# Optimization experiments

Measured on AMD Instinct MI355X. Metric: run time of the kernel, lower is better.

The kernel has to match this reference:

```python
import jax, jax.numpy as jnp
import numpy as np

L, B, D = 512, 32, 256  # seq_len, batch (hardcoded 32 in source), in_size == hidden_size
H = D


def setup_inputs() -> dict:
    key = jax.random.key(0)
    ks = jax.random.split(key, 9)
    s_in = 1.0 / np.sqrt(D)
    s_h = 1.0 / np.sqrt(H)
    return {
        "v": jax.random.normal(ks[0], (L, B, D), jnp.float32),
        "h0": jax.random.normal(ks[1], (B, H), jnp.float32),       # torch.randn h
        "Vvec": jax.random.normal(ks[2], (B, H), jnp.float32),     # torch.randn V (squeezed [B,H,1])
        "Wp": jax.random.normal(ks[3], (H, D), jnp.float32) * s_in,   # nn.Linear(D,H,bias=False).weight
        "Wp_": jax.random.normal(ks[4], (H, D), jnp.float32) * s_in,
        "W_ih": jax.random.normal(ks[5], (3 * H, D), jnp.float32) * s_h,  # GRUCell weight_ih
        "W_hh": jax.random.normal(ks[6], (3 * H, H), jnp.float32) * s_h,
        "b_ih": jax.random.normal(ks[7], (3 * H,), jnp.float32) * s_h,
        "b_hh": jax.random.normal(ks[8], (3 * H,), jnp.float32) * s_h,
    }


def _gru_cell(c, h, W_ih, W_hh, b_ih, b_hh):
    # torch.nn.GRUCell math
    gi = c @ W_ih.T + b_ih   # [B, 3H]
    gh = h @ W_hh.T + b_hh   # [B, 3H]
    i_r, i_z, i_n = jnp.split(gi, 3, axis=1)
    h_r, h_z, h_n = jnp.split(gh, 3, axis=1)
    r = jax.nn.sigmoid(i_r + h_r)
    z = jax.nn.sigmoid(i_z + h_z)
    n = jnp.tanh(i_n + r * h_n)
    return (1.0 - z) * n + z * h


def reference(v, h0, Vvec, Wp, Wp_, W_ih, W_hh, b_ih, b_hh):
    # Hoist the two linear projections out of the scan (they don't depend on h).
    xq = jnp.einsum('lbd,hd->lbh', v, Wp)    # Wp(v[i]) for all i
    xv = jnp.einsum('lbd,hd->lbh', v, Wp_)   # Wp_(v), reused every step

    def step(h, xq_i):
        x = jnp.tanh(xq_i[None, :, :] + xv)          # [L, B, H]
        s = jnp.einsum('lbh,bh->bl', x, Vvec)        # attention scores over L
        a = jax.nn.softmax(s, axis=1)                # [B, L]
        c = jnp.einsum('bl,lbd->bd', a, v)           # context [B, D]
        h_new = _gru_cell(c, h, W_ih, W_hh, b_ih, b_hh)
        return h_new, h_new

    _, hs = jax.lax.scan(step, h0, xq)  # hs: [L, B, H]
    # dropout is identity in eval mode
    return hs
```

## Files before the change

kernel.cpp:

```cpp
#include <hip/hip_runtime.h>
#include <stdint.h>


#define C2    2.8853900817779268f
#define LOG2E 1.4426950408889634f

typedef __fp16 f16x2 __attribute__((ext_vector_type(2)));
typedef __fp16 f16x4_t __attribute__((ext_vector_type(4)));
typedef __fp16 f16x8 __attribute__((ext_vector_type(8)));
typedef float f32x4 __attribute__((ext_vector_type(4)));

static __device__ __forceinline__ float rcp_f(float x)  { return __builtin_amdgcn_rcpf(x); }
static __device__ __forceinline__ float exp2_f(float x) { return __builtin_amdgcn_exp2f(x); }
#if __has_builtin(__builtin_amdgcn_rcph)
static __device__ __forceinline__ __fp16 rcph(__fp16 x) {
  return (__fp16)__builtin_amdgcn_rcph((_Float16)x);
}
#else
static __device__ __forceinline__ __fp16 rcph(__fp16 x) {
  return (__fp16)__builtin_amdgcn_rcpf((float)x);
}
#endif
static __device__ __forceinline__ float dot2f(f16x2 a, f16x2 b, float c) {
  return __builtin_amdgcn_fdot2(a, b, c, false);
}
static __device__ __forceinline__ f16x8 cvt8(float4 a, float4 b) {
  f16x8 f;
  f[0] = (__fp16)a.x; f[1] = (__fp16)a.y; f[2] = (__fp16)a.z; f[3] = (__fp16)a.w;
  f[4] = (__fp16)b.x; f[5] = (__fp16)b.y; f[6] = (__fp16)b.z; f[7] = (__fp16)b.w;
  return f;
}


__global__ __launch_bounds__(256) void proj_k(
    const float* __restrict__ v, const float* __restrict__ Wp,
    const float* __restrict__ Wp_, __fp16* __restrict__ Eq,
    __fp16* __restrict__ Ev)
{
  __shared__ __align__(16) __fp16 As[64][40];
  __shared__ __align__(16) __fp16 Wqs[64][40];
  __shared__ __align__(16) __fp16 Wvs[64][40];
  const int t = threadIdx.x, wave = t >> 6, lane = t & 63;
  const int quad = lane >> 4, col = lane & 15;
  const int n0 = blockIdx.x * 64, m0 = blockIdx.y * 64;
  const int srow = t >> 2, skq = t & 3;

  f32x4 accq[4], accv[4];
#pragma unroll
  for (int nt = 0; nt < 4; ++nt) {
    accq[nt] = (f32x4){0.f, 0.f, 0.f, 0.f};
    accv[nt] = (f32x4){0.f, 0.f, 0.f, 0.f};
  }

  for (int kc = 0; kc < 8; ++kc) {
    const int k0 = kc * 32;
    {
      const float4* ap = (const float4*)&v[(size_t)(m0 + srow) * 256 + k0 + skq * 8];
      *(f16x8*)&As[srow][skq * 8] = cvt8(ap[0], ap[1]);
      const float4* qp = (const float4*)&Wp[(size_t)(n0 + srow) * 256 + k0 + skq * 8];
      *(f16x8*)&Wqs[srow][skq * 8] = cvt8(qp[0], qp[1]);
      const float4* vp = (const float4*)&Wp_[(size_t)(n0 + srow) * 256 + k0 + skq * 8];
      *(f16x8*)&Wvs[srow][skq * 8] = cvt8(vp[0], vp[1]);
    }
    __syncthreads();
    f16x8 a = *(const f16x8*)&As[wave * 16 + col][quad * 8];
#pragma unroll
    for (int nt = 0; nt < 4; ++nt) {
      f16x8 bq = *(const f16x8*)&Wqs[nt * 16 + col][quad * 8];
      f16x8 bv = *(const f16x8*)&Wvs[nt * 16 + col][quad * 8];
      accq[nt] = __builtin_amdgcn_mfma_f32_16x16x32_f16(a, bq, accq[nt], 0, 0, 0);
      accv[nt] = __builtin_amdgcn_mfma_f32_16x16x32_f16(a, bv, accv[nt], 0, 0, 0);
    }
    __syncthreads();
  }

#pragma unroll
  for (int nt = 0; nt < 4; ++nt)
#pragma unroll
    for (int r = 0; r < 4; ++r) {
      size_t m = m0 + wave * 16 + quad * 4 + r;
      size_t n = n0 + nt * 16 + col;
      float eq = C2 * accq[nt][r], ev = C2 * accv[nt][r];
      eq = fminf(fmaxf(eq, -14.f), 15.5f);
      ev = fminf(fmaxf(ev, -14.f), 15.5f);
      Eq[m * 256 + n] = (__fp16)exp2_f(eq);
      Ev[m * 256 + n] = (__fp16)exp2_f(ev);
    }
}

__global__ __launch_bounds__(256) void score_k(
    const __fp16* __restrict__ Eq, const __fp16* __restrict__ Ev,
    const float* __restrict__ Vvec, float* __restrict__ S)
{
  __shared__ __align__(16) __fp16 Eqs[64][72];
  __shared__ __align__(16) __fp16 Evs[32][72];
  __shared__ __align__(16) __fp16 Vs[256];
  const int t = threadIdx.x;
  const int tx = t & 15, ty = t >> 4;
  const int l0 = blockIdx.x * 32;
  const int i0 = blockIdx.y * 64;
  const int b  = blockIdx.z;

  Vs[t] = (__fp16)(-2.0f * Vvec[b * 256 + t]);
  float acc[4][2] = {};
  const f16x2 one2 = {(__fp16)1.f, (__fp16)1.f};

  for (int st = 0; st < 4; ++st) {
    const int h0 = st * 64;
#pragma unroll
    for (int s = 0; s < 2; ++s) {
      int f = t + s * 256;
      int row = f >> 3, cq = f & 7;
      *(f16x8*)&Eqs[row][cq * 8] =
          *(const f16x8*)&Eq[((size_t)(i0 + row) * 32 + b) * 256 + h0 + cq * 8];
    }
    {
      int row = t >> 3, cq = t & 7;
      *(f16x8*)&Evs[row][cq * 8] =
          *(const f16x8*)&Ev[((size_t)(l0 + row) * 32 + b) * 256 + h0 + cq * 8];
    }
    __syncthreads();

#pragma unroll
    for (int k8 = 0; k8 < 8; ++k8) {
      f16x8 vh8 = *(const f16x8*)&Vs[h0 + k8 * 8];
      f16x8 ev80 = *(const f16x8*)&Evs[tx][k8 * 8];
      f16x8 ev81 = *(const f16x8*)&Evs[tx + 16][k8 * 8];
      f16x8 eq8[4];
#pragma unroll
      for (int r = 0; r < 4; ++r)
        eq8[r] = *(const f16x8*)&Eqs[ty * 4 + r][k8 * 8];
#pragma unroll
      for (int q = 0; q < 4; ++q) {
        f16x2 vh2 = {vh8[q * 2], vh8[q * 2 + 1]};
        f16x2 e0  = {ev80[q * 2], ev80[q * 2 + 1]};
        f16x2 e1  = {ev81[q * 2], ev81[q * 2 + 1]};
#pragma unroll
        for (int r = 0; r < 4; ++r) {
          f16x2 eq2 = {eq8[r][q * 2], eq8[r][q * 2 + 1]};
          f16x2 d0 = eq2 * e0 + one2;
          f16x2 d1 = eq2 * e1 + one2;
          f16x2 r0 = {rcph(d0[0]), rcph(d0[1])};
          f16x2 r1 = {rcph(d1[0]), rcph(d1[1])};
          acc[r][0] = dot2f(vh2, r0, acc[r][0]);
          acc[r][1] = dot2f(vh2, r1, acc[r][1]);
        }
      }
    }
    __syncthreads();
  }

#pragma unroll
  for (int r = 0; r < 4; ++r) {
    float* ps = &S[((size_t)b * 512 + i0 + ty * 4 + r) * 512 + l0];
    ps[tx]      = acc[r][0];
    ps[tx + 16] = acc[r][1];
  }
}

__global__ __launch_bounds__(256) void softmax_k(float* __restrict__ S)
{
  const int wave = threadIdx.x >> 6, lane = threadIdx.x & 63;
  float* row = &S[((size_t)blockIdx.x * 4 + wave) * 512];
  float4 x0 = *(float4*)&row[lane * 4];
  float4 x1 = *(float4*)&row[256 + lane * 4];
  float m = fmaxf(fmaxf(fmaxf(x0.x, x0.y), fmaxf(x0.z, x0.w)),
                  fmaxf(fmaxf(x1.x, x1.y), fmaxf(x1.z, x1.w)));
#pragma unroll
  for (int o = 32; o; o >>= 1) m = fmaxf(m, __shfl_xor(m, o, 64));
  x0.x = exp2_f(LOG2E * (x0.x - m)); x0.y = exp2_f(LOG2E * (x0.y - m));
  x0.z = exp2_f(LOG2E * (x0.z - m)); x0.w = exp2_f(LOG2E * (x0.w - m));
  x1.x = exp2_f(LOG2E * (x1.x - m)); x1.y = exp2_f(LOG2E * (x1.y - m));
  x1.z = exp2_f(LOG2E * (x1.z - m)); x1.w = exp2_f(LOG2E * (x1.w - m));
  float sum = x0.x + x0.y + x0.z + x0.w + x1.x + x1.y + x1.z + x1.w;
#pragma unroll
  for (int o = 32; o; o >>= 1) sum += __shfl_xor(sum, o, 64);
  float inv = rcp_f(sum);
  x0.x *= inv; x0.y *= inv; x0.z *= inv; x0.w *= inv;
  x1.x *= inv; x1.y *= inv; x1.z *= inv; x1.w *= inv;
  *(float4*)&row[lane * 4] = x0;
  *(float4*)&row[256 + lane * 4] = x1;
}

__global__ __launch_bounds__(256) void ctxm_k(
    const float* __restrict__ Aw, const float* __restrict__ v,
    float* __restrict__ C)
{
  __shared__ __align__(16) __fp16 As[64][40];
  __shared__ __align__(16) __fp16 Vs[64][40];
  const int t = threadIdx.x, wave = t >> 6, lane = t & 63;
  const int quad = lane >> 4, col = lane & 15;
  const int d0 = blockIdx.x * 64, i0 = blockIdx.y * 64, b = blockIdx.z;
  const int srow = t >> 2, skq = t & 3;
  const int vl = t >> 3, vdq = t & 7;

  f32x4 acc[4];
#pragma unroll
  for (int nt = 0; nt < 4; ++nt) acc[nt] = (f32x4){0.f, 0.f, 0.f, 0.f};

  for (int kc = 0; kc < 16; ++kc) {
    const int l0 = kc * 32;
    {
      const float4* ap =
          (const float4*)&Aw[((size_t)b * 512 + i0 + srow) * 512 + l0 + skq * 8];
      *(f16x8*)&As[srow][skq * 8] = cvt8(ap[0], ap[1]);
      const float4* vp =
          (const float4*)&v[((size_t)(l0 + vl) * 32 + b) * 256 + d0 + vdq * 8];
      float4 v0 = vp[0], v1 = vp[1];
      float vv[8] = {v0.x, v0.y, v0.z, v0.w, v1.x, v1.y, v1.z, v1.w};
#pragma unroll
      for (int e = 0; e < 8; ++e) Vs[vdq * 8 + e][vl] = (__fp16)vv[e];
    }
    __syncthreads();
    f16x8 a = *(const f16x8*)&As[wave * 16 + col][quad * 8];
#pragma unroll
    for (int nt = 0; nt < 4; ++nt) {
      f16x8 bb = *(const f16x8*)&Vs[nt * 16 + col][quad * 8];
      acc[nt] = __builtin_amdgcn_mfma_f32_16x16x32_f16(a, bb, acc[nt], 0, 0, 0);
    }
    __syncthreads();
  }

#pragma unroll
  for (int nt = 0; nt < 4; ++nt)
#pragma unroll
    for (int r = 0; r < 4; ++r) {
      size_t i = i0 + wave * 16 + quad * 4 + r;
      size_t d = d0 + nt * 16 + col;
      C[(i * 32 + b) * 256 + d] = acc[nt][r];
    }
}

__global__ __launch_bounds__(256) void gi_k(
    const float* __restrict__ A, const float* __restrict__ W,
    const float* __restrict__ bih, const float* __restrict__ bhh,
    __fp16* __restrict__ G)
{
  __shared__ __align__(16) __fp16 As[64][40];
  __shared__ __align__(16) __fp16 Ws[64][40];
  const int t = threadIdx.x, wave = t >> 6, lane = t & 63;
  const int quad = lane >> 4, col = lane & 15;
  const int n0 = blockIdx.x * 64, m0 = blockIdx.y * 64;
  const int srow = t >> 2, skq = t & 3;

  f32x4 acc[4];
#pragma unroll
  for (int nt = 0; nt < 4; ++nt) acc[nt] = (f32x4){0.f, 0.f, 0.f, 0.f};

  for (int kc = 0; kc < 8; ++kc) {
    const int k0 = kc * 32;
    {
      const float4* ap = (const float4*)&A[(size_t)(m0 + srow) * 256 + k0 + skq * 8];
      *(f16x8*)&As[srow][skq * 8] = cvt8(ap[0], ap[1]);
      const float4* wp = (const float4*)&W[(size_t)(n0 + srow) * 256 + k0 + skq * 8];
      *(f16x8*)&Ws[srow][skq * 8] = cvt8(wp[0], wp[1]);
    }
    __syncthreads();
    f16x8 a = *(const f16x8*)&As[wave * 16 + col][quad * 8];
#pragma unroll
    for (int nt = 0; nt < 4; ++nt) {
      f16x8 b = *(const f16x8*)&Ws[nt * 16 + col][quad * 8];
      acc[nt] = __builtin_amdgcn_mfma_f32_16x16x32_f16(a, b, acc[nt], 0, 0, 0);
    }
    __syncthreads();
  }

#pragma unroll
  for (int nt = 0; nt < 4; ++nt) {
    int n = n0 + nt * 16 + col;
    float bias = bih[n] + (n < 512 ? bhh[n] : 0.f);
#pragma unroll
    for (int r = 0; r < 4; ++r) {
      size_t m = m0 + wave * 16 + quad * 4 + r;
      G[m * 768 + n] = (__fp16)(acc[nt][r] + bias);
    }
  }
}

__global__ __launch_bounds__(512, 1) void gru_k(
    const __fp16* __restrict__ Gi2, const float* __restrict__ Whh,
    const float* __restrict__ bhh, const float* __restrict__ h0,
    float* __restrict__ out)
{
  __shared__ __align__(16) __fp16 hA[2][256];
  const int t = threadIdx.x, wave = t >> 6, lane = t & 63;
  const int quad = lane >> 4, col = lane & 15;
  const int b = blockIdx.x;
  const int jw = wave * 32;

  f16x8 Bf[2][3][8];
#pragma unroll
  for (int p = 0; p < 2; ++p)
#pragma unroll
    for (int g = 0; g < 3; ++g) {
      const float* wrow = &Whh[(size_t)(g * 256 + jw + p * 16 + col) * 256];
#pragma unroll
      for (int kk = 0; kk < 8; ++kk) {
        const float4* wp = (const float4*)&wrow[kk * 32 + quad * 8];
        Bf[p][g][kk] = cvt8(wp[0], wp[1]);
      }
    }

  float hold[2];
  float bn[2];
#pragma unroll
  for (int p = 0; p < 2; ++p) {
    int j = jw + p * 16 + col;
    bn[p] = bhh[512 + j];
    float h = h0[(size_t)b * 256 + j];
    hold[p] = h;
    if (quad == 0) hA[0][j] = (__fp16)h;
  }
  __syncthreads();

  __fp16 gcur[2][3];
#pragma unroll
  for (int p = 0; p < 2; ++p)
#pragma unroll
    for (int g = 0; g < 3; ++g)
      gcur[p][g] = Gi2[(size_t)b * 768 + g * 256 + jw + p * 16 + col];

  for (int i = 0; i < 512; ++i) {
    __fp16 gnext[2][3];
    {
      int ip = (i + 1 < 512) ? (i + 1) : 511;
#pragma unroll
      for (int p = 0; p < 2; ++p)
#pragma unroll
        for (int g = 0; g < 3; ++g)
          gnext[p][g] =
              Gi2[(size_t)(ip * 32 + b) * 768 + g * 256 + jw + p * 16 + col];
    }

    f32x4 acc[2][3];
#pragma unroll
    for (int p = 0; p < 2; ++p)
#pragma unroll
      for (int g = 0; g < 3; ++g)
        acc[p][g] = (f32x4){0.f, 0.f, 0.f, 0.f};

    const __fp16* hbuf = hA[i & 1];
#pragma unroll
    for (int kk = 0; kk < 8; ++kk) {
      f16x8 a = *(const f16x8*)&hbuf[kk * 32 + quad * 8];
#pragma unroll
      for (int p = 0; p < 2; ++p)
#pragma unroll
        for (int g = 0; g < 3; ++g)
          acc[p][g] = __builtin_amdgcn_mfma_f32_16x16x32_f16(
              a, Bf[p][g][kk], acc[p][g], 0, 0, 0);
    }

    __fp16* hnext = hA[(i + 1) & 1];
#pragma unroll
    for (int p = 0; p < 2; ++p) {
      int j = jw + p * 16 + col;
      float rr = rcp_f(1.f + exp2_f(-LOG2E * ((float)gcur[p][0] + acc[p][0][0])));
      float zz = rcp_f(1.f + exp2_f(-LOG2E * ((float)gcur[p][1] + acc[p][1][0])));
      float na = fmaf(rr, acc[p][2][0] + bn[p], (float)gcur[p][2]);
      float nn = fmaf(-2.f, rcp_f(1.f + exp2_f(C2 * na)), 1.f);
      float h = fmaf(zz, hold[p] - nn, nn);
      hold[p] = h;
      if (quad == 0) {
        out[((size_t)i * 32 + b) * 256 + j] = h;
        hnext[j] = (__fp16)h;
      }
    }
#pragma unroll
    for (int p = 0; p < 2; ++p)
#pragma unroll
      for (int g = 0; g < 3; ++g) gcur[p][g] = gnext[p][g];
    __syncthreads();
  }
}

extern "C" void kernel_launch(void* const* d_in, const int* in_sizes, int n_in,
                              void* d_out, int out_size, void* d_ws, size_t ws_size,
                              hipStream_t stream)
{
  const float* v   = (const float*)d_in[0];
  const float* h0  = (const float*)d_in[1];
  const float* Vv  = (const float*)d_in[2];
  const float* Wp  = (const float*)d_in[3];
  const float* Wp_ = (const float*)d_in[4];
  const float* Wih = (const float*)d_in[5];
  const float* Whh = (const float*)d_in[6];
  const float* bih = (const float*)d_in[7];
  const float* bhh = (const float*)d_in[8];
  float* out = (float*)d_out;
  float* ws  = (float*)d_ws;

  __fp16* Eq = (__fp16*)ws;
  __fp16* Ev = (__fp16*)(ws + 4194304);
  float*  S  = ws + 8388608;
  float*  C  = ws;
  __fp16* Gi2 = (__fp16*)(ws + 4194304);

  proj_k<<<dim3(4, 256), 256, 0, stream>>>(v, Wp, Wp_, Eq, Ev);
  score_k<<<dim3(16, 8, 32), 256, 0, stream>>>(Eq, Ev, Vv, S);
  softmax_k<<<4096, 256, 0, stream>>>(S);
  ctxm_k<<<dim3(4, 8, 32), 256, 0, stream>>>(S, v, C);
  gi_k<<<dim3(12, 256), 256, 0, stream>>>(C, Wih, bih, bhh, Gi2);
  gru_k<<<32, 512, 0, stream>>>(Gi2, Whh, bhh, h0, out);
}
```

Before: 921.2 us.

## Fuse score, softmax and context matmul into one attention kernel

Replaces the separate score, softmax and context kernels with a single attn_k in which each block of 512 threads computes scores for 64 query rows against all 512 keys. It applies the softmax in registers with shuffles, stages the probabilities in fp16 shared memory, and runs the context MFMA matmul over the whole D. This removes the 32 MB fp32 score matrix round trip through global memory and two kernel launches, and the context is now written as fp16 for gi_k. The cost is a grid of only 256 blocks with launch_bounds(512,1), a heavy register load from 64 accumulators per thread, large shared memory and reduced occupancy.

```diff
diff --git a/kernel.cpp b/kernel.cpp
--- a/kernel.cpp
+++ b/kernel.cpp
@@ -6,7 +6,6 @@
 #define LOG2E 1.4426950408889634f
 
 typedef __fp16 f16x2 __attribute__((ext_vector_type(2)));
-typedef __fp16 f16x4_t __attribute__((ext_vector_type(4)));
 typedef __fp16 f16x8 __attribute__((ext_vector_type(8)));
 typedef float f32x4 __attribute__((ext_vector_type(4)));
 
@@ -88,62 +87,68 @@
     }
 }
 
-__global__ __launch_bounds__(256) void score_k(
+__global__ __launch_bounds__(512, 1) void attn_k(
     const __fp16* __restrict__ Eq, const __fp16* __restrict__ Ev,
-    const float* __restrict__ Vvec, float* __restrict__ S)
-{
-  __shared__ __align__(16) __fp16 Eqs[64][72];
-  __shared__ __align__(16) __fp16 Evs[32][72];
-  __shared__ __align__(16) __fp16 Vs[256];
+    const float* __restrict__ Vvec, const float* __restrict__ v,
+    __fp16* __restrict__ C)
+{
+  __shared__ __align__(16) __fp16 smem[43520];
+  __shared__ __align__(16) __fp16 Vsh[256];
   const int t = threadIdx.x;
-  const int tx = t & 15, ty = t >> 4;
-  const int l0 = blockIdx.x * 32;
-  const int i0 = blockIdx.y * 64;
-  const int b  = blockIdx.z;
-
-  Vs[t] = (__fp16)(-2.0f * Vvec[b * 256 + t]);
-  float acc[4][2] = {};
+  const int tx = t & 31, ty = t >> 5;
+  const int wave = t >> 6, lane = t & 63;
+  const int quad = lane >> 4, col = lane & 15;
+  const int i0 = blockIdx.x * 64, b = blockIdx.y;
+
+  if (t < 256) Vsh[t] = (__fp16)(-2.0f * Vvec[b * 256 + t]);
+
+  float acc[16][4];
+#pragma unroll
+  for (int lt = 0; lt < 16; ++lt)
+#pragma unroll
+    for (int r = 0; r < 4; ++r) acc[lt][r] = 0.f;
+
+  __fp16* Eqs = smem;
+  __fp16* Evs = smem + 4608;
   const f16x2 one2 = {(__fp16)1.f, (__fp16)1.f};
 
   for (int st = 0; st < 4; ++st) {
     const int h0 = st * 64;
-#pragma unroll
-    for (int s = 0; s < 2; ++s) {
-      int f = t + s * 256;
+    {
+      int row = t >> 3, cq = t & 7;
+      *(f16x8*)&Eqs[row * 72 + cq * 8] =
+          *(const f16x8*)&Eq[((size_t)(i0 + row) * 32 + b) * 256 + h0 + cq * 8];
+    }
+#pragma unroll
+    for (int s = 0; s < 8; ++s) {
+      int f = t + s * 512;
       int row = f >> 3, cq = f & 7;
-      *(f16x8*)&Eqs[row][cq * 8] =
-          *(const f16x8*)&Eq[((size_t)(i0 + row) * 32 + b) * 256 + h0 + cq * 8];
-    }
-    {
-      int row = t >> 3, cq = t & 7;
-      *(f16x8*)&Evs[row][cq * 8] =
-          *(const f16x8*)&Ev[((size_t)(l0 + row) * 32 + b) * 256 + h0 + cq * 8];
-    }
-    __syncthreads();
-
-#pragma unroll
-    for (int k8 = 0; k8 < 8; ++k8) {
-      f16x8 vh8 = *(const f16x8*)&Vs[h0 + k8 * 8];
-      f16x8 ev80 = *(const f16x8*)&Evs[tx][k8 * 8];
-      f16x8 ev81 = *(const f16x8*)&Evs[tx + 16][k8 * 8];
-      f16x8 eq8[4];
-#pragma unroll
-      for (int r = 0; r < 4; ++r)
-        eq8[r] = *(const f16x8*)&Eqs[ty * 4 + r][k8 * 8];
-#pragma unroll
-      for (int q = 0; q < 4; ++q) {
-        f16x2 vh2 = {vh8[q * 2], vh8[q * 2 + 1]};
-        f16x2 e0  = {ev80[q * 2], ev80[q * 2 + 1]};
-        f16x2 e1  = {ev81[q * 2], ev81[q * 2 + 1]};
-#pragma unroll
-        for (int r = 0; r < 4; ++r) {
-          f16x2 eq2 = {eq8[r][q * 2], eq8[r][q * 2 + 1]};
-          f16x2 d0 = eq2 * e0 + one2;
-          f16x2 d1 = eq2 * e1 + one2;
-          f16x2 r0 = {rcph(d0[0]), rcph(d0[1])};
-          f16x2 r1 = {rcph(d1[0]), rcph(d1[1])};
-          acc[r][0] = dot2f(vh2, r0, acc[r][0]);
-          acc[r][1] = dot2f(vh2, r1, acc[r][1]);
+      *(f16x8*)&Evs[row * 72 + cq * 8] =
+          *(const f16x8*)&Ev[((size_t)row * 32 + b) * 256 + h0 + cq * 8];
+    }
+    __syncthreads();
+
+#pragma unroll
+    for (int lt = 0; lt < 16; ++lt) {
+#pragma unroll
+      for (int k8 = 0; k8 < 8; ++k8) {
+        f16x8 vh8 = *(const f16x8*)&Vsh[h0 + k8 * 8];
+        f16x8 ev8 = *(const f16x8*)&Evs[(lt * 32 + tx) * 72 + k8 * 8];
+        f16x8 eq8[4];
+#pragma unroll
+        for (int r = 0; r < 4; ++r)
+          eq8[r] = *(const f16x8*)&Eqs[(ty * 4 + r) * 72 + k8 * 8];
+#pragma unroll
+        for (int q = 0; q < 4; ++q) {
+          f16x2 vh2 = {vh8[q * 2], vh8[q * 2 + 1]};
+          f16x2 e2  = {ev8[q * 2], ev8[q * 2 + 1]};
+#pragma unroll
+          for (int r = 0; r < 4; ++r) {
+            f16x2 eq2 = {eq8[r][q * 2], eq8[r][q * 2 + 1]};
+            f16x2 d = eq2 * e2 + one2;
+            f16x2 rr = {rcph(d[0]), rcph(d[1])};
+            acc[lt][r] = dot2f(vh2, rr, acc[lt][r]);
+          }
         }
       }
     }
@@ -152,87 +157,75 @@
 
 #pragma unroll
   for (int r = 0; r < 4; ++r) {
-    float* ps = &S[((size_t)b * 512 + i0 + ty * 4 + r) * 512 + l0];
-    ps[tx]      = acc[r][0];
-    ps[tx + 16] = acc[r][1];
-  }
-}
-
-__global__ __launch_bounds__(256) void softmax_k(float* __restrict__ S)
-{
-  const int wave = threadIdx.x >> 6, lane = threadIdx.x & 63;
-  float* row = &S[((size_t)blockIdx.x * 4 + wave) * 512];
-  float4 x0 = *(float4*)&row[lane * 4];
-  float4 x1 = *(float4*)&row[256 + lane * 4];
-  float m = fmaxf(fmaxf(fmaxf(x0.x, x0.y), fmaxf(x0.z, x0.w)),
-                  fmaxf(fmaxf(x1.x, x1.y), fmaxf(x1.z, x1.w)));
-#pragma unroll
-  for (int o = 32; o; o >>= 1) m = fmaxf(m, __shfl_xor(m, o, 64));
-  x0.x = exp2_f(LOG2E * (x0.x - m)); x0.y = exp2_f(LOG2E * (x0.y - m));
-  x0.z = exp2_f(LOG2E * (x0.z - m)); x0.w = exp2_f(LOG2E * (x0.w - m));
-  x1.x = exp2_f(LOG2E * (x1.x - m)); x1.y = exp2_f(LOG2E * (x1.y - m));
-  x1.z = exp2_f(LOG2E * (x1.z - m)); x1.w = exp2_f(LOG2E * (x1.w - m));
-  float sum = x0.x + x0.y + x0.z + x0.w + x1.x + x1.y + x1.z + x1.w;
-#pragma unroll
-  for (int o = 32; o; o >>= 1) sum += __shfl_xor(sum, o, 64);
-  float inv = rcp_f(sum);
-  x0.x *= inv; x0.y *= inv; x0.z *= inv; x0.w *= inv;
-  x1.x *= inv; x1.y *= inv; x1.z *= inv; x1.w *= inv;
-  *(float4*)&row[lane * 4] = x0;
-  *(float4*)&row[256 + lane * 4] = x1;
-}
-
-__global__ __launch_bounds__(256) void ctxm_k(
-    const float* __restrict__ Aw, const float* __restrict__ v,
-    float* __restrict__ C)
-{
-  __shared__ __align__(16) __fp16 As[64][40];
-  __shared__ __align__(16) __fp16 Vs[64][40];
-  const int t = threadIdx.x, wave = t >> 6, lane = t & 63;
-  const int quad = lane >> 4, col = lane & 15;
-  const int d0 = blockIdx.x * 64, i0 = blockIdx.y * 64, b = blockIdx.z;
-  const int srow = t >> 2, skq = t & 3;
-  const int vl = t >> 3, vdq = t & 7;
-
-  f32x4 acc[4];
-#pragma unroll
-  for (int nt = 0; nt < 4; ++nt) acc[nt] = (f32x4){0.f, 0.f, 0.f, 0.f};
+    float m = -1e30f;
+#pragma unroll
+    for (int lt = 0; lt < 16; ++lt) m = fmaxf(m, acc[lt][r]);
+#pragma unroll
+    for (int o = 1; o < 32; o <<= 1) m = fmaxf(m, __shfl_xor(m, o, 64));
+    float s = 0.f;
+#pragma unroll
+    for (int lt = 0; lt < 16; ++lt) {
+      acc[lt][r] = exp2_f(LOG2E * (acc[lt][r] - m));
+      s += acc[lt][r];
+    }
+#pragma unroll
+    for (int o = 1; o < 32; o <<= 1) s += __shfl_xor(s, o, 64);
+    float inv = rcp_f(s);
+#pragma unroll
+    for (int lt = 0; lt < 16; ++lt) acc[lt][r] *= inv;
+  }
+
+  __fp16* Af = smem;
+#pragma unroll
+  for (int r = 0; r < 4; ++r)
+#pragma unroll
+    for (int lt = 0; lt < 16; ++lt)
+      Af[(ty * 4 + r) * 520 + lt * 32 + tx] = (__fp16)acc[lt][r];
+  __syncthreads();
+
+  __fp16* Vs = smem + 33280;
+  const int mt = wave & 3, nh = wave >> 2;
+  const int vl = t >> 4, vdq = t & 15;
+  f32x4 acc2[8];
+#pragma unroll
+  for (int n = 0; n < 8; ++n) acc2[n] = (f32x4){0.f, 0.f, 0.f, 0.f};
 
   for (int kc = 0; kc < 16; ++kc) {
     const int l0 = kc * 32;
     {
-      const float4* ap =
-          (const float4*)&Aw[((size_t)b * 512 + i0 + srow) * 512 + l0 + skq * 8];
-      *(f16x8*)&As[srow][skq * 8] = cvt8(ap[0], ap[1]);
       const float4* vp =
-          (const float4*)&v[((size_t)(l0 + vl) * 32 + b) * 256 + d0 + vdq * 8];
-      float4 v0 = vp[0], v1 = vp[1];
-      float vv[8] = {v0.x, v0.y, v0.z, v0.w, v1.x, v1.y, v1.z, v1.w};
-#pragma unroll
-      for (int e = 0; e < 8; ++e) Vs[vdq * 8 + e][vl] = (__fp16)vv[e];
-    }
-    __syncthreads();
-    f16x8 a = *(const f16x8*)&As[wave * 16 + col][quad * 8];
-#pragma unroll
-    for (int nt = 0; nt < 4; ++nt) {
-      f16x8 bb = *(const f16x8*)&Vs[nt * 16 + col][quad * 8];
-      acc[nt] = __builtin_amdgcn_mfma_f32_16x16x32_f16(a, bb, acc[nt], 0, 0, 0);
-    }
-    __syncthreads();
-  }
-
-#pragma unroll
-  for (int nt = 0; nt < 4; ++nt)
+          (const float4*)&v[((size_t)(l0 + vl) * 32 + b) * 256 + vdq * 16];
+#pragma unroll
+      for (int e4 = 0; e4 < 4; ++e4) {
+        float4 w = vp[e4];
+        Vs[(vdq * 16 + e4 * 4 + 0) * 40 + vl] = (__fp16)w.x;
+        Vs[(vdq * 16 + e4 * 4 + 1) * 40 + vl] = (__fp16)w.y;
+        Vs[(vdq * 16 + e4 * 4 + 2) * 40 + vl] = (__fp16)w.z;
+        Vs[(vdq * 16 + e4 * 4 + 3) * 40 + vl] = (__fp16)w.w;
+      }
+    }
+    __syncthreads();
+    f16x8 af = *(const f16x8*)&Af[(mt * 16 + col) * 520 + l0 + quad * 8];
+#pragma unroll
+    for (int n = 0; n < 8; ++n) {
+      f16x8 vf = *(const f16x8*)&Vs[((nh * 8 + n) * 16 + col) * 40 + quad * 8];
+      acc2[n] = __builtin_amdgcn_mfma_f32_16x16x32_f16(af, vf, acc2[n], 0, 0, 0);
+    }
+    __syncthreads();
+  }
+
+#pragma unroll
+  for (int n = 0; n < 8; ++n)
 #pragma unroll
     for (int r = 0; r < 4; ++r) {
-      size_t i = i0 + wave * 16 + quad * 4 + r;
-      size_t d = d0 + nt * 16 + col;
-      C[(i * 32 + b) * 256 + d] = acc[nt][r];
+      size_t i = i0 + mt * 16 + quad * 4 + r;
+      size_t d = (nh * 8 + n) * 16 + col;
+      C[(i * 32 + b) * 256 + d] = (__fp16)acc2[n][r];
     }
 }
 
 __global__ __launch_bounds__(256) void gi_k(
-    const float* __restrict__ A, const float* __restrict__ W,
+    const __fp16* __restrict__ A, const float* __restrict__ W,
     const float* __restrict__ bih, const float* __restrict__ bhh,
     __fp16* __restrict__ G)
 {
@@ -250,8 +243,8 @@
   for (int kc = 0; kc < 8; ++kc) {
     const int k0 = kc * 32;
     {
-      const float4* ap = (const float4*)&A[(size_t)(m0 + srow) * 256 + k0 + skq * 8];
-      *(f16x8*)&As[srow][skq * 8] = cvt8(ap[0], ap[1]);
+      *(f16x8*)&As[srow][skq * 8] =
+          *(const f16x8*)&A[(size_t)(m0 + srow) * 256 + k0 + skq * 8];
       const float4* wp = (const float4*)&W[(size_t)(n0 + srow) * 256 + k0 + skq * 8];
       *(f16x8*)&Ws[srow][skq * 8] = cvt8(wp[0], wp[1]);
     }
@@ -390,16 +383,13 @@
   float* out = (float*)d_out;
   float* ws  = (float*)d_ws;
 
-  __fp16* Eq = (__fp16*)ws;
-  __fp16* Ev = (__fp16*)(ws + 4194304);
-  float*  S  = ws + 8388608;
-  float*  C  = ws;
-  __fp16* Gi2 = (__fp16*)(ws + 4194304);
+  __fp16* Eq  = (__fp16*)ws;
+  __fp16* Ev  = (__fp16*)(ws + 2097152);
+  __fp16* C   = (__fp16*)(ws + 4194304);
+  __fp16* Gi2 = (__fp16*)(ws + 6291456);
 
   proj_k<<<dim3(4, 256), 256, 0, stream>>>(v, Wp, Wp_, Eq, Ev);
-  score_k<<<dim3(16, 8, 32), 256, 0, stream>>>(Eq, Ev, Vv, S);
-  softmax_k<<<4096, 256, 0, stream>>>(S);
-  ctxm_k<<<dim3(4, 8, 32), 256, 0, stream>>>(S, v, C);
+  attn_k<<<dim3(8, 32), 512, 0, stream>>>(Eq, Ev, Vv, v, C);
   gi_k<<<dim3(12, 256), 256, 0, stream>>>(C, Wih, bih, bhh, Gi2);
   gru_k<<<32, 512, 0, stream>>>(Gi2, Whh, bhh, h0, out);
 }
```

After: 976.9 us. +6.1%, slower.
